# Kernel optimization log

Measured on AMD Instinct MI355X. Metric: run time of the kernel, lower is better.

## Reference

```python
import jax, jax.numpy as jnp
import numpy as np

N = 50000      # nodes
F = 256        # num_features
H = 128        # hidden_size
R = 16         # num_relations
E = 800000     # edges
C = 7          # num_classes
NB = 30        # num_bases (hard-coded in module)


def setup_inputs() -> dict:
    key = jax.random.key(0)
    ks = jax.random.split(key, 16)
    g = lambda k, shape, fan_in: jax.random.normal(k, shape, jnp.float32) / np.float32(np.sqrt(fan_in))
    inp = {
        "x": jax.random.normal(ks[0], (N, F), jnp.float32),
        "edge_index": jax.random.randint(ks[1], (2, E), 0, N),
        "edge_norm": jax.random.uniform(ks[2], (E,), jnp.float32),
        "edge_type": jax.random.randint(ks[3], (E,), 0, R),
        "seq_lengths": jax.random.randint(ks[4], (16,), 1, 100),
        "umask": jnp.ones((16, 110), jnp.float32),
        "nodal_attn": 0,
        "avec": 0,
        # RGCNConv (basis decomposition)
        "basis": g(ks[5], (NB, F, H), F),
        "comp": g(ks[6], (R, NB), NB),
        "root1": g(ks[7], (F, H), F),
        "bias1": jnp.zeros((H,), jnp.float32),
        # GraphConv
        "w_rel": g(ks[8], (H, H), H),
        "w_root": g(ks[9], (H, H), H),
        "bias2": jnp.zeros((H,), jnp.float32),
        # classification head
        "lin_w": g(ks[10], (F + H, H), F + H),
        "lin_b": jnp.zeros((H,), jnp.float32),
        "fc_w": g(ks[11], (H, C), H),
        "fc_b": jnp.zeros((C,), jnp.float32),
    }
    return inp


def reference(x, edge_index, edge_norm, edge_type, seq_lengths, umask,
              nodal_attn, avec, basis, comp, root1, bias1,
              w_rel, w_root, bias2, lin_w, lin_b, fc_w, fc_b):
    src, dst = edge_index[0], edge_index[1]

    # ---- RGCNConv: basis-decomposed relational conv, mean aggr per relation ----
    W = jnp.einsum('rb,bio->rio', comp, basis)          # [R,F,H]
    xW = jnp.einsum('ni,rio->nro', x, W)                # [N,R,H]
    msgs = xW[src, edge_type]                           # [E,H]
    seg = dst * R + edge_type                           # (dst, relation) segment id
    cnt = jax.ops.segment_sum(jnp.ones((E,), jnp.float32), seg, num_segments=N * R)
    inv = 1.0 / jnp.maximum(cnt, 1.0)
    agg1 = jax.ops.segment_sum(msgs * inv[seg][:, None], dst, num_segments=N)
    out1 = agg1 + x @ root1 + bias1                     # [N,H]

    # ---- GraphConv: sum aggr + root transform ----
    agg2 = jax.ops.segment_sum(out1[src], dst, num_segments=N)  # [N,H]
    out2 = agg2 @ w_rel + bias2 + out1 @ w_root         # [N,H]

    # ---- classification head (nodal_attn=False path; dropout is identity in eval) ----
    emotions = jnp.concatenate([x, out2], axis=-1)      # [N,F+H]
    hidden = jax.nn.relu(emotions @ lin_w + lin_b)      # [N,H]
    logits = hidden @ fc_w + fc_b                       # [N,C]
    return jax.nn.log_softmax(logits, axis=1)
```

## Files before the change

kernel.cpp:

```cpp
#include <hip/hip_runtime.h>
#include <hip/hip_bf16.h>
#include <stdint.h>

#define NN 50000
#define FF 256
#define HH 128
#define RR 16
#define EE 800000
#define CC 7
#define NB_ 30

typedef __attribute__((ext_vector_type(8))) short short8;
typedef __attribute__((ext_vector_type(4))) float f32x4;

__device__ __forceinline__ float bf2f(unsigned short u){
  union { unsigned int i; float f; } x; x.i = ((unsigned int)u) << 16; return x.f;
}
__device__ __forceinline__ unsigned short f2bf(float f){
  union { unsigned int i; float f; } x; x.f = f;
  unsigned int r = x.i + 0x7fffu + ((x.i >> 16) & 1u);
  return (unsigned short)(r >> 16);
}

__device__ __forceinline__ void gld16(const unsigned short* g, unsigned short* l){
  __builtin_amdgcn_global_load_lds(
      (const __attribute__((address_space(1))) unsigned int*)g,
      (__attribute__((address_space(3))) unsigned int*)l, 16, 0, 0);
}

template<bool BIAS, bool RELU>
__global__ __launch_bounds__(256) void gemm_bt(
    const unsigned short* __restrict__ A0, int ldA0,
    const unsigned short* __restrict__ A1, int ldA1, int kSplit,
    const unsigned short* __restrict__ Bt,
    unsigned short* __restrict__ Cout, int ldC,
    const float* __restrict__ bias,
    int M, int K)
{
  __shared__ unsigned short Al[128*64];
  __shared__ unsigned short Bl[128*64];
  const int tid  = threadIdx.x;
  const int lane = tid & 63;
  const int wid  = tid >> 6;
  const int wr   = wid >> 1, wc = wid & 1;
  const int bm   = blockIdx.x, bn = blockIdx.y;

  f32x4 acc[4][4];
  #pragma unroll
  for (int m=0;m<4;m++)
    #pragma unroll
    for (int n=0;n<4;n++) acc[m][n] = (f32x4){0.f,0.f,0.f,0.f};

  const int nkt = K >> 6;
  for (int kt=0; kt<nkt; ++kt){
    int c0 = kt*64;
    const unsigned short* Asrc = A0; int lda = ldA0;
    if (c0 >= kSplit){ Asrc = A1; lda = ldA1; c0 -= kSplit; }
    const unsigned short* arow = Asrc + (size_t)(bm*128 + wid*32 + (lane>>3))*lda + c0 + (lane&7)*8;
    const unsigned short* brow = Bt   + (size_t)(bn*128 + wid*32 + (lane>>3))*K  + kt*64 + (lane&7)*8;
    #pragma unroll
    for (int i=0;i<4;i++){
      gld16(arow + (size_t)i*8*lda, &Al[(wid*32 + i*8)*64]);
      gld16(brow + (size_t)i*8*K,   &Bl[(wid*32 + i*8)*64]);
    }
    __syncthreads();
    #pragma unroll
    for (int ks=0; ks<2; ++ks){
      short8 a[4], b[4];
      #pragma unroll
      for (int m=0;m<4;m++)
        a[m] = *(const short8*)&Al[(wr*64 + m*16 + (lane&15))*64 + ks*32 + (lane>>4)*8];
      #pragma unroll
      for (int n=0;n<4;n++)
        b[n] = *(const short8*)&Bl[(wc*64 + n*16 + (lane&15))*64 + ks*32 + (lane>>4)*8];
      #pragma unroll
      for (int m=0;m<4;m++)
        #pragma unroll
        for (int n=0;n<4;n++)
          acc[m][n] = __builtin_amdgcn_mfma_f32_16x16x32_bf16(a[m], b[n], acc[m][n], 0, 0, 0);
    }
    __syncthreads();
  }

  #pragma unroll
  for (int m=0;m<4;m++){
    #pragma unroll
    for (int n=0;n<4;n++){
      #pragma unroll
      for (int j=0;j<4;j++){
        int row = bm*128 + wr*64 + m*16 + ((lane>>4)<<2) + j;
        int col = bn*128 + wc*64 + n*16 + (lane&15);
        if (row < M){
          float v = acc[m][n][j];
          if (BIAS) v += bias[col];
          if (RELU) v = fmaxf(v, 0.f);
          Cout[(size_t)row*ldC + col] = f2bf(v);
        }
      }
    }
  }
}

__global__ void k_cvt(const float* __restrict__ in, unsigned short* __restrict__ out, int n4){
  int i = blockIdx.x*256 + threadIdx.x;
  if (i >= n4) return;
  float4 v = ((const float4*)in)[i];
  union { unsigned short u[4]; uint2 q; } t;
  t.u[0]=f2bf(v.x); t.u[1]=f2bf(v.y); t.u[2]=f2bf(v.z); t.u[3]=f2bf(v.w);
  ((uint2*)out)[i] = t.q;
}

__global__ __launch_bounds__(256) void k_build_wt(const float* __restrict__ comp,
                                                  const float* __restrict__ basis,
                                                  unsigned short* __restrict__ WT){
  __shared__ float sm[16][129];
  __shared__ float cmp[NB_];
  int r = blockIdx.x >> 4, i0 = (blockIdx.x & 15)*16;
  int o = threadIdx.x & 127, ih = threadIdx.x >> 7;
  if (threadIdx.x < NB_) cmp[threadIdx.x] = comp[r*NB_ + threadIdx.x];
  __syncthreads();
  #pragma unroll
  for (int step=0; step<8; ++step){
    int i = i0 + step*2 + ih;
    float s = 0.f;
    #pragma unroll 6
    for (int b=0;b<NB_;b++) s += cmp[b]*basis[((size_t)b*FF + i)*HH + o];
    sm[step*2+ih][o] = s;
  }
  __syncthreads();
  #pragma unroll
  for (int w=0;w<8;w++){
    int o2 = w*16 + (threadIdx.x>>4);
    int ii = threadIdx.x & 15;
    WT[((size_t)(r*128 + o2))*FF + i0 + ii] = f2bf(sm[ii][o2]);
  }
}

__global__ void k_transpose_cat(const float* __restrict__ in0, int k0,
                                const float* __restrict__ in1, int k1,
                                unsigned short* __restrict__ outT){
  int K = k0 + k1;
  int idx = blockIdx.x*256 + threadIdx.x;
  if (idx >= 128*K) return;
  int o = idx / K, k = idx % K;
  float v = (k < k0) ? in0[(size_t)k*HH + o] : in1[(size_t)(k-k0)*HH + o];
  outT[idx] = f2bf(v);
}

__global__ void k_count(const int* __restrict__ dstv, int* __restrict__ counts){
  int e = blockIdx.x*256 + threadIdx.x;
  if (e >= EE) return;
  atomicAdd(&counts[dstv[e]], 1);
}

__global__ __launch_bounds__(256) void k_scan1(const int* __restrict__ counts,
                                               int* __restrict__ row_ptr,
                                               int* __restrict__ blocksum){
  __shared__ int wsum[4];
  int g = blockIdx.x*256 + threadIdx.x;
  int lane = threadIdx.x & 63, wv = threadIdx.x >> 6;
  int v = (g < NN) ? counts[g] : 0;
  int s = v;
  #pragma unroll
  for (int off=1; off<64; off<<=1){ int t = __shfl_up(s, off, 64); if (lane>=off) s += t; }
  if (lane==63) wsum[wv] = s;
  __syncthreads();
  int wo = 0;
  #pragma unroll
  for (int i=0;i<4;i++) if (i < wv) wo += wsum[i];
  int incl = s + wo;
  if (g < NN) row_ptr[g] = incl - v;
  if (threadIdx.x == 255) blocksum[blockIdx.x] = incl;
}
__global__ __launch_bounds__(256) void k_scan2(int* __restrict__ blocksum, int nb){
  __shared__ int wsum[4];
  int t = threadIdx.x, lane = t & 63, wv = t >> 6;
  int v = (t < nb) ? blocksum[t] : 0;
  int s = v;
  #pragma unroll
  for (int off=1; off<64; off<<=1){ int u = __shfl_up(s, off, 64); if (lane>=off) s += u; }
  if (lane==63) wsum[wv] = s;
  __syncthreads();
  int wo = 0;
  #pragma unroll
  for (int i=0;i<4;i++) if (i < wv) wo += wsum[i];
  if (t < nb) blocksum[t] = s + wo - v;
}
__global__ __launch_bounds__(256) void k_scan3(int* __restrict__ row_ptr,
                                               const int* __restrict__ blocksum){
  int g = blockIdx.x*256 + threadIdx.x;
  if (g < NN) row_ptr[g] += blocksum[blockIdx.x];
  if (g == 0) row_ptr[NN] = EE;
}

__global__ void k_fill(const int* __restrict__ srcv, const int* __restrict__ dstv,
                       const int* __restrict__ etv, const int* __restrict__ row_ptr,
                       int* __restrict__ cursor, int* __restrict__ packed){
  int e = blockIdx.x*256 + threadIdx.x;
  if (e >= EE) return;
  int d = dstv[e];
  int p = atomicAdd(&cursor[d], 1);
  packed[row_ptr[d] + p] = (srcv[e] & 0xffff) | (etv[e] << 16);
}

__global__ __launch_bounds__(256) void k_agg1(const int* __restrict__ row_ptr,
                                              const int* __restrict__ packed,
                                              const unsigned int* __restrict__ xWu,
                                              unsigned int* __restrict__ out1u){
  __shared__ int   cnt[4][RR];
  __shared__ float inv[4][RR];
  const int lane = threadIdx.x & 63;
  const int wv   = threadIdx.x >> 6;
  const int node = blockIdx.x*4 + wv;
  if (lane < RR) cnt[wv][lane] = 0;
  __syncthreads();
  const int b0 = row_ptr[node], b1 = row_ptr[node+1];
  for (int j=b0+lane; j<b1; j+=64) atomicAdd(&cnt[wv][(packed[j]>>16)&15], 1);
  __syncthreads();
  if (lane < RR) inv[wv][lane] = 1.0f / fmaxf((float)cnt[wv][lane], 1.0f);
  __syncthreads();

  float aA0=0.f, aA1=0.f, aB0=0.f, aB1=0.f;
  int j = b0;
  for (; j+4 <= b1; j+=4){
    int p0=packed[j], p1=packed[j+1], p2=packed[j+2], p3=packed[j+3];
    unsigned int v0 = xWu[((size_t)(((p0&0xffff)<<4)|((p0>>16)&15)) << 6) + lane];
    unsigned int v1 = xWu[((size_t)(((p1&0xffff)<<4)|((p1>>16)&15)) << 6) + lane];
    unsigned int v2 = xWu[((size_t)(((p2&0xffff)<<4)|((p2>>16)&15)) << 6) + lane];
    unsigned int v3 = xWu[((size_t)(((p3&0xffff)<<4)|((p3>>16)&15)) << 6) + lane];
    float i0=inv[wv][(p0>>16)&15], i1=inv[wv][(p1>>16)&15];
    float i2=inv[wv][(p2>>16)&15], i3=inv[wv][(p3>>16)&15];
    aA0 += bf2f((unsigned short)v0)*i0; aA1 += bf2f((unsigned short)(v0>>16))*i0;
    aB0 += bf2f((unsigned short)v1)*i1; aB1 += bf2f((unsigned short)(v1>>16))*i1;
    aA0 += bf2f((unsigned short)v2)*i2; aA1 += bf2f((unsigned short)(v2>>16))*i2;
    aB0 += bf2f((unsigned short)v3)*i3; aB1 += bf2f((unsigned short)(v3>>16))*i3;
  }
  for (; j<b1; ++j){
    int p = packed[j];
    unsigned int v = xWu[((size_t)(((p&0xffff)<<4)|((p>>16)&15)) << 6) + lane];
    float iv = inv[wv][(p>>16)&15];
    aA0 += bf2f((unsigned short)v)*iv; aA1 += bf2f((unsigned short)(v>>16))*iv;
  }
  size_t o = (size_t)node*64 + lane;
  unsigned int cur = out1u[o];
  float r0 = bf2f((unsigned short)cur)       + aA0 + aB0;
  float r1 = bf2f((unsigned short)(cur>>16)) + aA1 + aB1;
  out1u[o] = (unsigned int)f2bf(r0) | ((unsigned int)f2bf(r1) << 16);
}

__global__ __launch_bounds__(256) void k_agg2(const int* __restrict__ row_ptr,
                                              const int* __restrict__ packed,
                                              const unsigned int* __restrict__ out1u,
                                              unsigned int* __restrict__ agg2u){
  const int lane = threadIdx.x & 63;
  const int wv   = threadIdx.x >> 6;
  const int node = blockIdx.x*4 + wv;
  const int b0 = row_ptr[node], b1 = row_ptr[node+1];
  float aA0=0.f, aA1=0.f, aB0=0.f, aB1=0.f;
  int j = b0;
  for (; j+4 <= b1; j+=4){
    int p0=packed[j]&0xffff, p1=packed[j+1]&0xffff, p2=packed[j+2]&0xffff, p3=packed[j+3]&0xffff;
    unsigned int v0 = out1u[(size_t)p0*64 + lane];
    unsigned int v1 = out1u[(size_t)p1*64 + lane];
    unsigned int v2 = out1u[(size_t)p2*64 + lane];
    unsigned int v3 = out1u[(size_t)p3*64 + lane];
    aA0 += bf2f((unsigned short)v0); aA1 += bf2f((unsigned short)(v0>>16));
    aB0 += bf2f((unsigned short)v1); aB1 += bf2f((unsigned short)(v1>>16));
    aA0 += bf2f((unsigned short)v2); aA1 += bf2f((unsigned short)(v2>>16));
    aB0 += bf2f((unsigned short)v3); aB1 += bf2f((unsigned short)(v3>>16));
  }
  for (; j<b1; ++j){
    unsigned int v = out1u[(size_t)(packed[j]&0xffff)*64 + lane];
    aA0 += bf2f((unsigned short)v); aA1 += bf2f((unsigned short)(v>>16));
  }
  agg2u[(size_t)node*64 + lane] = (unsigned int)f2bf(aA0+aB0) | ((unsigned int)f2bf(aA1+aB1) << 16);
}

__global__ __launch_bounds__(256) void k_head(const unsigned short* __restrict__ hidden,
                                              const float* __restrict__ fc_w,
                                              const float* __restrict__ fc_b,
                                              float* __restrict__ out){
  int node = blockIdx.x*4 + (threadIdx.x >> 6);
  int lane = threadIdx.x & 63;
  if (node >= NN) return;
  float h0 = bf2f(hidden[(size_t)node*128 + lane*2]);
  float h1 = bf2f(hidden[(size_t)node*128 + lane*2 + 1]);
  float lg[CC];
  #pragma unroll
  for (int c=0;c<CC;c++){
    float p = h0*fc_w[(lane*2)*CC + c] + h1*fc_w[(lane*2+1)*CC + c];
    #pragma unroll
    for (int off=32; off; off>>=1) p += __shfl_down(p, off, 64);
    lg[c] = p;
  }
  if (lane == 0){
    float l[CC]; float m = -1e30f;
    #pragma unroll
    for (int c=0;c<CC;c++){ l[c] = lg[c] + fc_b[c]; m = fmaxf(m, l[c]); }
    float s = 0.f;
    #pragma unroll
    for (int c=0;c<CC;c++) s += expf(l[c]-m);
    float lse = logf(s);
    #pragma unroll
    for (int c=0;c<CC;c++) out[(size_t)node*CC + c] = l[c] - m - lse;
  }
}

extern "C" void kernel_launch(void* const* d_in, const int* in_sizes, int n_in,
                              void* d_out, int out_size, void* d_ws, size_t ws_size,
                              hipStream_t stream)
{
  const float* x      = (const float*)d_in[0];
  const int*   eidx   = (const int*)d_in[1];
  const int*   etype  = (const int*)d_in[3];
  const float* basis  = (const float*)d_in[8];
  const float* comp   = (const float*)d_in[9];
  const float* root1  = (const float*)d_in[10];
  const float* bias1  = (const float*)d_in[11];
  const float* w_rel  = (const float*)d_in[12];
  const float* w_root = (const float*)d_in[13];
  const float* bias2  = (const float*)d_in[14];
  const float* lin_w  = (const float*)d_in[15];
  const float* lin_b  = (const float*)d_in[16];
  const float* fc_w   = (const float*)d_in[17];
  const float* fc_b   = (const float*)d_in[18];
  const int* srcv = eidx;
  const int* dstv = eidx + EE;

  char* w = (char*)d_ws;
  unsigned short* x_bf    = (unsigned short*)(w + 0);
  unsigned short* xW      = (unsigned short*)(w + 25624576);
  unsigned short* hidden  = (unsigned short*)(w + 25624576);
  unsigned short* out2_bf = (unsigned short*)(w + 25624576 + 12812288);
  unsigned short* agg2_bf = (unsigned short*)(w + 25624576 + 25624576);
  unsigned short* WT      = (unsigned short*)(w + 230424576);
  unsigned short* rootT   = (unsigned short*)(w + 231473152);
  unsigned short* W2T     = (unsigned short*)(w + 231538688);
  unsigned short* linT    = (unsigned short*)(w + 231604224);
  unsigned short* out1_bf = (unsigned short*)(w + 231702528);
  int*            counts  = (int*)(w + 244514816);
  int*            row_ptr = (int*)(w + 244715008);
  int*            cursor  = (int*)(w + 244915200);
  int*            packed  = (int*)(w + 245115392);
  int*            blocksum= (int*)(w + 248315392);

  hipMemsetAsync(counts, 0, NN*4, stream);
  hipMemsetAsync(cursor, 0, NN*4, stream);

  k_cvt<<<12500, 256, 0, stream>>>(x, x_bf, NN*FF/4);
  k_build_wt<<<256, 256, 0, stream>>>(comp, basis, WT);
  k_transpose_cat<<<128, 256, 0, stream>>>(root1, 256, nullptr, 0, rootT);
  k_transpose_cat<<<128, 256, 0, stream>>>(w_rel, 128, w_root, 128, W2T);
  k_transpose_cat<<<192, 256, 0, stream>>>(lin_w, 384, nullptr, 0, linT);

  k_count<<<3125, 256, 0, stream>>>(dstv, counts);
  k_scan1<<<196, 256, 0, stream>>>(counts, row_ptr, blocksum);
  k_scan2<<<1, 256, 0, stream>>>(blocksum, 196);
  k_scan3<<<196, 256, 0, stream>>>(row_ptr, blocksum);
  k_fill<<<3125, 256, 0, stream>>>(srcv, dstv, etype, row_ptr, cursor, packed);

  {
    dim3 g(391, 16);
    gemm_bt<false,false><<<g, 256, 0, stream>>>(
        x_bf, FF, nullptr, 0, 1<<30, WT, xW, 2048, nullptr, NN, FF);
  }
  {
    dim3 g(391, 1);
    gemm_bt<true,false><<<g, 256, 0, stream>>>(
        x_bf, FF, nullptr, 0, 1<<30, rootT, out1_bf, HH, bias1, NN, FF);
  }
  k_agg1<<<12500, 256, 0, stream>>>(row_ptr, packed, (const unsigned int*)xW, (unsigned int*)out1_bf);
  k_agg2<<<12500, 256, 0, stream>>>(row_ptr, packed, (const unsigned int*)out1_bf, (unsigned int*)agg2_bf);
  {
    dim3 g(391, 1);
    gemm_bt<true,false><<<g, 256, 0, stream>>>(
        agg2_bf, HH, out1_bf, HH, HH, W2T, out2_bf, HH, bias2, NN, 2*HH);
  }
  {
    dim3 g(391, 1);
    gemm_bt<true,true><<<g, 256, 0, stream>>>(
        x_bf, FF, out2_bf, HH, FF, linT, hidden, HH, lin_b, NN, FF+HH);
  }
  k_head<<<12500, 256, 0, stream>>>(hidden, fc_w, fc_b, (float*)d_out);
}
```

Baseline: 421.5 us.

## Raster GEMM blocks by XCD, vectorize epilogue stores, deepen gather unroll

The big xW GEMM now launches on a 1D grid. Each block index is remapped so that consecutive blocks on the same XCD walk all 16 column tiles of a group of 8 row tiles, which should improve L2 reuse of the A tiles. The MFMA operands are swapped so that each lane holds 4 consecutive columns, letting the epilogue write packed 8-byte bf16 stores instead of scattered 2-byte stores. The edge gather loops in agg1 and agg2 are unrolled to 8 outstanding loads, with two accumulators instead of four, to raise memory-level parallelism.

```diff
diff --git a/kernel.cpp b/kernel.cpp
--- a/kernel.cpp
+++ b/kernel.cpp
@@ -28,7 +28,7 @@
       (__attribute__((address_space(3))) unsigned int*)l, 16, 0, 0);
 }
 
-template<bool BIAS, bool RELU>
+template<bool BIAS, bool RELU, bool RASTER>
 __global__ __launch_bounds__(256) void gemm_bt(
     const unsigned short* __restrict__ A0, int ldA0,
     const unsigned short* __restrict__ A1, int ldA1, int kSplit,
@@ -43,7 +43,18 @@
   const int lane = tid & 63;
   const int wid  = tid >> 6;
   const int wr   = wid >> 1, wc = wid & 1;
-  const int bm   = blockIdx.x, bn = blockIdx.y;
+  int bm, bn;
+  if (RASTER){
+    int idx  = blockIdx.x;
+    int cidx = (idx & 7)*782 + (idx >> 3);
+    int p = cidx >> 7;
+    int within = cidx & 127;
+    int ph = min(8, 391 - p*8);
+    bn = within / ph;
+    bm = p*8 + within % ph;
+  } else {
+    bm = blockIdx.x; bn = blockIdx.y;
+  }
 
   f32x4 acc[4][4];
   #pragma unroll
@@ -77,25 +88,24 @@
       for (int m=0;m<4;m++)
         #pragma unroll
         for (int n=0;n<4;n++)
-          acc[m][n] = __builtin_amdgcn_mfma_f32_16x16x32_bf16(a[m], b[n], acc[m][n], 0, 0, 0);
+          acc[m][n] = __builtin_amdgcn_mfma_f32_16x16x32_bf16(b[n], a[m], acc[m][n], 0, 0, 0);
     }
     __syncthreads();
   }
 
   #pragma unroll
   for (int m=0;m<4;m++){
-    #pragma unroll
-    for (int n=0;n<4;n++){
+    int row = bm*128 + wr*64 + m*16 + (lane&15);
+    if (row < M){
       #pragma unroll
-      for (int j=0;j<4;j++){
-        int row = bm*128 + wr*64 + m*16 + ((lane>>4)<<2) + j;
-        int col = bn*128 + wc*64 + n*16 + (lane&15);
-        if (row < M){
-          float v = acc[m][n][j];
-          if (BIAS) v += bias[col];
-          if (RELU) v = fmaxf(v, 0.f);
-          Cout[(size_t)row*ldC + col] = f2bf(v);
-        }
+      for (int n=0;n<4;n++){
+        int col = bn*128 + wc*64 + n*16 + ((lane>>4)<<2);
+        float v0 = acc[m][n][0], v1 = acc[m][n][1], v2 = acc[m][n][2], v3 = acc[m][n][3];
+        if (BIAS){ v0 += bias[col]; v1 += bias[col+1]; v2 += bias[col+2]; v3 += bias[col+3]; }
+        if (RELU){ v0 = fmaxf(v0,0.f); v1 = fmaxf(v1,0.f); v2 = fmaxf(v2,0.f); v3 = fmaxf(v3,0.f); }
+        unsigned int lo = (unsigned int)f2bf(v0) | ((unsigned int)f2bf(v1) << 16);
+        unsigned int hi = (unsigned int)f2bf(v2) | ((unsigned int)f2bf(v3) << 16);
+        *(uint2*)&Cout[(size_t)row*ldC + col] = make_uint2(lo, hi);
       }
     }
   }
@@ -220,31 +230,47 @@
   if (lane < RR) inv[wv][lane] = 1.0f / fmaxf((float)cnt[wv][lane], 1.0f);
   __syncthreads();
 
-  float aA0=0.f, aA1=0.f, aB0=0.f, aB1=0.f;
+  float a0=0.f, a1=0.f;
   int j = b0;
+  for (; j+8 <= b1; j+=8){
+    int pv[8]; unsigned int vv[8];
+    #pragma unroll
+    for (int q=0;q<8;q++) pv[q] = packed[j+q];
+    #pragma unroll
+    for (int q=0;q<8;q++)
+      vv[q] = xWu[((size_t)(((pv[q]&0xffff)<<4)|((pv[q]>>16)&15)) << 6) + lane];
+    #pragma unroll
+    for (int q=0;q<8;q++){
+      float f = inv[wv][(pv[q]>>16)&15];
+      a0 += bf2f((unsigned short)vv[q])*f;
+      a1 += bf2f((unsigned short)(vv[q]>>16))*f;
+    }
+  }
   for (; j+4 <= b1; j+=4){
-    int p0=packed[j], p1=packed[j+1], p2=packed[j+2], p3=packed[j+3];
-    unsigned int v0 = xWu[((size_t)(((p0&0xffff)<<4)|((p0>>16)&15)) << 6) + lane];
-    unsigned int v1 = xWu[((size_t)(((p1&0xffff)<<4)|((p1>>16)&15)) << 6) + lane];
-    unsigned int v2 = xWu[((size_t)(((p2&0xffff)<<4)|((p2>>16)&15)) << 6) + lane];
-    unsigned int v3 = xWu[((size_t)(((p3&0xffff)<<4)|((p3>>16)&15)) << 6) + lane];
-    float i0=inv[wv][(p0>>16)&15], i1=inv[wv][(p1>>16)&15];
-    float i2=inv[wv][(p2>>16)&15], i3=inv[wv][(p3>>16)&15];
-    aA0 += bf2f((unsigned short)v0)*i0; aA1 += bf2f((unsigned short)(v0>>16))*i0;
-    aB0 += bf2f((unsigned short)v1)*i1; aB1 += bf2f((unsigned short)(v1>>16))*i1;
-    aA0 += bf2f((unsigned short)v2)*i2; aA1 += bf2f((unsigned short)(v2>>16))*i2;
-    aB0 += bf2f((unsigned short)v3)*i3; aB1 += bf2f((unsigned short)(v3>>16))*i3;
+    int pv[4]; unsigned int vv[4];
+    #pragma unroll
+    for (int q=0;q<4;q++) pv[q] = packed[j+q];
+    #pragma unroll
+    for (int q=0;q<4;q++)
+      vv[q] = xWu[((size_t)(((pv[q]&0xffff)<<4)|((pv[q]>>16)&15)) << 6) + lane];
+    #pragma unroll
+    for (int q=0;q<4;q++){
+      float f = inv[wv][(pv[q]>>16)&15];
+      a0 += bf2f((unsigned short)vv[q])*f;
+      a1 += bf2f((unsigned short)(vv[q]>>16))*f;
+    }
   }
   for (; j<b1; ++j){
     int p = packed[j];
     unsigned int v = xWu[((size_t)(((p&0xffff)<<4)|((p>>16)&15)) << 6) + lane];
-    float iv = inv[wv][(p>>16)&15];
-    aA0 += bf2f((unsigned short)v)*iv; aA1 += bf2f((unsigned short)(v>>16))*iv;
+    float f = inv[wv][(p>>16)&15];
+    a0 += bf2f((unsigned short)v)*f;
+    a1 += bf2f((unsigned short)(v>>16))*f;
   }
   size_t o = (size_t)node*64 + lane;
   unsigned int cur = out1u[o];
-  float r0 = bf2f((unsigned short)cur)       + aA0 + aB0;
-  float r1 = bf2f((unsigned short)(cur>>16)) + aA1 + aB1;
+  float r0 = bf2f((unsigned short)cur)       + a0;
+  float r1 = bf2f((unsigned short)(cur>>16)) + a1;
   out1u[o] = (unsigned int)f2bf(r0) | ((unsigned int)f2bf(r1) << 16);
 }
 
@@ -256,24 +282,36 @@
   const int wv   = threadIdx.x >> 6;
   const int node = blockIdx.x*4 + wv;
   const int b0 = row_ptr[node], b1 = row_ptr[node+1];
-  float aA0=0.f, aA1=0.f, aB0=0.f, aB1=0.f;
+  float a0=0.f, a1=0.f;
   int j = b0;
+  for (; j+8 <= b1; j+=8){
+    unsigned int vv[8];
+    #pragma unroll
+    for (int q=0;q<8;q++)
+      vv[q] = out1u[(size_t)(packed[j+q]&0xffff)*64 + lane];
+    #pragma unroll
+    for (int q=0;q<8;q++){
+      a0 += bf2f((unsigned short)vv[q]);
+      a1 += bf2f((unsigned short)(vv[q]>>16));
+    }
+  }
   for (; j+4 <= b1; j+=4){
-    int p0=packed[j]&0xffff, p1=packed[j+1]&0xffff, p2=packed[j+2]&0xffff, p3=packed[j+3]&0xffff;
-    unsigned int v0 = out1u[(size_t)p0*64 + lane];
-    unsigned int v1 = out1u[(size_t)p1*64 + lane];
-    unsigned int v2 = out1u[(size_t)p2*64 + lane];
-    unsigned int v3 = out1u[(size_t)p3*64 + lane];
-    aA0 += bf2f((unsigned short)v0); aA1 += bf2f((unsigned short)(v0>>16));
-    aB0 += bf2f((unsigned short)v1); aB1 += bf2f((unsigned short)(v1>>16));
-    aA0 += bf2f((unsigned short)v2); aA1 += bf2f((unsigned short)(v2>>16));
-    aB0 += bf2f((unsigned short)v3); aB1 += bf2f((unsigned short)(v3>>16));
+    unsigned int vv[4];
+    #pragma unroll
+    for (int q=0;q<4;q++)
+      vv[q] = out1u[(size_t)(packed[j+q]&0xffff)*64 + lane];
+    #pragma unroll
+    for (int q=0;q<4;q++){
+      a0 += bf2f((unsigned short)vv[q]);
+      a1 += bf2f((unsigned short)(vv[q]>>16));
+    }
   }
   for (; j<b1; ++j){
     unsigned int v = out1u[(size_t)(packed[j]&0xffff)*64 + lane];
-    aA0 += bf2f((unsigned short)v); aA1 += bf2f((unsigned short)(v>>16));
-  }
-  agg2u[(size_t)node*64 + lane] = (unsigned int)f2bf(aA0+aB0) | ((unsigned int)f2bf(aA1+aB1) << 16);
+    a0 += bf2f((unsigned short)v);
+    a1 += bf2f((unsigned short)(v>>16));
+  }
+  agg2u[(size_t)node*64 + lane] = (unsigned int)f2bf(a0) | ((unsigned int)f2bf(a1) << 16);
 }
 
 __global__ __launch_bounds__(256) void k_head(const unsigned short* __restrict__ hidden,
@@ -359,26 +397,23 @@
   k_scan3<<<196, 256, 0, stream>>>(row_ptr, blocksum);
   k_fill<<<3125, 256, 0, stream>>>(srcv, dstv, etype, row_ptr, cursor, packed);
 
-  {
-    dim3 g(391, 16);
-    gemm_bt<false,false><<<g, 256, 0, stream>>>(
-        x_bf, FF, nullptr, 0, 1<<30, WT, xW, 2048, nullptr, NN, FF);
-  }
+  gemm_bt<false,false,true><<<6256, 256, 0, stream>>>(
+      x_bf, FF, nullptr, 0, 1<<30, WT, xW, 2048, nullptr, NN, FF);
   {
     dim3 g(391, 1);
-    gemm_bt<true,false><<<g, 256, 0, stream>>>(
+    gemm_bt<true,false,false><<<g, 256, 0, stream>>>(
         x_bf, FF, nullptr, 0, 1<<30, rootT, out1_bf, HH, bias1, NN, FF);
   }
   k_agg1<<<12500, 256, 0, stream>>>(row_ptr, packed, (const unsigned int*)xW, (unsigned int*)out1_bf);
   k_agg2<<<12500, 256, 0, stream>>>(row_ptr, packed, (const unsigned int*)out1_bf, (unsigned int*)agg2_bf);
   {
     dim3 g(391, 1);
-    gemm_bt<true,false><<<g, 256, 0, stream>>>(
+    gemm_bt<true,false,false><<<g, 256, 0, stream>>>(
         agg2_bf, HH, out1_bf, HH, HH, W2T, out2_bf, HH, bias2, NN, 2*HH);
   }
   {
     dim3 g(391, 1);
-    gemm_bt<true,true><<<g, 256, 0, stream>>>(
+    gemm_bt<true,true,false><<<g, 256, 0, stream>>>(
         x_bf, FF, out2_bf, HH, FF, linT, hidden, HH, lin_b, NN, FF+HH);
   }
   k_head<<<12500, 256, 0, stream>>>(hidden, fc_w, fc_b, (float*)d_out);
```

New measurement: 408.0 us (median of 2 runs). 3.2% less time.
